# Performance work log

Measured on AMD Instinct MI355X. Metric: run time of the kernel, lower is better.

## Reference

```python
import jax, jax.numpy as jnp
import numpy as np

B, S, H = 2, 2048, 4096
NUM_HEADS = 32
HEAD_DIM = H // NUM_HEADS  # 128
ROPE_BASE = 10000.0


def _apply_rope(x, positions):
    # x: [B, S, nh, hd]; neox-style (half-split) rotation, rotary_dim == head_dim
    hd = x.shape[-1]
    inv_freq = 1.0 / (ROPE_BASE ** (jnp.arange(0, hd, 2, dtype=jnp.float32) / hd))  # [hd/2]
    freqs = positions[..., None].astype(jnp.float32) * inv_freq  # [B, S, hd/2]
    cos = jnp.cos(freqs)[:, :, None, :].astype(x.dtype)
    sin = jnp.sin(freqs)[:, :, None, :].astype(x.dtype)
    x1, x2 = jnp.split(x, 2, axis=-1)
    return jnp.concatenate([x1 * cos - x2 * sin, x2 * cos + x1 * sin], axis=-1)


def setup_inputs() -> dict:
    key = jax.random.key(0)
    k1, k2, k3 = jax.random.split(key, 3)
    hidden_states = jax.random.normal(k1, (B, S, H), dtype=jnp.float32) * 0.02
    positions = jnp.broadcast_to(jnp.arange(S, dtype=jnp.int32), (B, S))
    w_pack = jax.random.normal(k2, (3 * H, H), dtype=jnp.float32) * 0.02  # Linear(H, 3H), no bias
    w_o = jax.random.normal(k3, (H, H), dtype=jnp.float32) * 0.02        # Linear(H, H), no bias
    return {"hidden_states": hidden_states, "w_pack": w_pack, "w_o": w_o, "positions": positions}


def reference(hidden_states, w_pack, w_o, positions):
    b, s, h = hidden_states.shape
    nh, hd = NUM_HEADS, HEAD_DIM
    # fused QKV projection (W_pack)
    qkv = hidden_states @ w_pack.T  # [B, S, 3H]
    q, k, v = jnp.split(qkv, 3, axis=-1)
    q = q.reshape(b, s, nh, hd)
    k = k.reshape(b, s, nh, hd)
    v = v.reshape(b, s, nh, hd)
    # RoPE on q and k
    q = _apply_rope(q, positions)
    k = _apply_rope(k, positions)
    # causal scaled-dot-product attention (prefill over full KV cache)
    scale = 1.0 / jnp.sqrt(jnp.asarray(hd, dtype=q.dtype))
    scores = jnp.einsum('bqhd,bkhd->bhqk', q, k) * scale  # [B, nh, S, S]
    causal = jnp.tril(jnp.ones((s, s), dtype=bool))
    neg = jnp.asarray(jnp.finfo(scores.dtype).min, dtype=scores.dtype)
    scores = jnp.where(causal[None, None], scores, neg)
    attn = jax.nn.softmax(scores, axis=-1)
    out = jnp.einsum('bhqk,bkhd->bqhd', attn, v).reshape(b, s, h)
    # output projection
    return out @ w_o.T
```

## Files before the change

### kernel.cpp

```cpp
#include <hip/hip_runtime.h>
#include <hip/hip_bf16.h>
#include <math.h>

#define B_    2
#define S_    2048
#define H_    4096
#define NH_   32
#define HD_   128
#define MTOK_ (B_ * S_)
#define QKVN_ (3 * H_)

using bf16_t = __hip_bfloat16;
typedef __bf16 bf16x8 __attribute__((ext_vector_type(8)));
typedef unsigned short u16x8 __attribute__((ext_vector_type(8)));
typedef float f32x4 __attribute__((ext_vector_type(4)));

#define ASYNC_COPY16(g, l)                                                     \
  __builtin_amdgcn_global_load_lds(                                            \
      (__attribute__((address_space(1))) void*)(g),                            \
      (__attribute__((address_space(3))) void*)(l), 16, 0, 0)

static __device__ __forceinline__ f32x4 mfma16x16(bf16x8 a, bf16x8 b, f32x4 c) {
  return __builtin_amdgcn_mfma_f32_16x16x32_bf16(a, b, c, 0, 0, 0);
}

static __device__ __forceinline__ float bits_to_f(unsigned short v) {
  union { unsigned int u; float f; } cv;
  cv.u = ((unsigned int)v) << 16;
  return cv.f;
}

#define GBAR()                                                                 \
  do {                                                                         \
    __builtin_amdgcn_s_barrier();                                              \
    __builtin_amdgcn_sched_barrier(0);                                         \
  } while (0)

#define LGKM0()                                                                \
  do {                                                                         \
    asm volatile("s_waitcnt lgkmcnt(0)" ::: "memory");                         \
    __builtin_amdgcn_sched_barrier(0);                                         \
  } while (0)

__global__ void bh_detect(const unsigned short* __restrict__ p,
                          int* __restrict__ flag) {
  __shared__ float red[4];
  float m = 0.f;
  const int tid = threadIdx.x;
  for (int i = tid; i < 65536; i += 256) {
    const float f = fabsf(bits_to_f(p[i]));
    m = fmaxf(m, f);
  }
  for (int off = 1; off < 64; off <<= 1) m = fmaxf(m, __shfl_xor(m, off, 64));
  if ((tid & 63) == 0) red[tid >> 6] = m;
  __syncthreads();
  if (tid == 0) {
    const float mm = fmaxf(fmaxf(red[0], red[1]), fmaxf(red[2], red[3]));
    *flag = (mm > 1.0f) ? 1 : 0;
  }
}

__global__ __launch_bounds__(256)
void bh_convert(const void* __restrict__ src, bf16_t* __restrict__ dst,
                long n8, const int* __restrict__ flag) {
  const int isf = *flag;
  const long stride = (long)gridDim.x * 256;
  long i = (long)blockIdx.x * 256 + threadIdx.x;
  if (isf) {
    const f32x4* s = (const f32x4*)src;
    for (; i < n8; i += stride) {
      const f32x4 f0 = s[2 * i];
      const f32x4 f1 = s[2 * i + 1];
      bf16x8 o;
      o[0] = (__bf16)f0[0]; o[1] = (__bf16)f0[1];
      o[2] = (__bf16)f0[2]; o[3] = (__bf16)f0[3];
      o[4] = (__bf16)f1[0]; o[5] = (__bf16)f1[1];
      o[6] = (__bf16)f1[2]; o[7] = (__bf16)f1[3];
      *reinterpret_cast<bf16x8*>(dst + i * 8) = o;
    }
  } else {
    const u16x8* s = (const u16x8*)src;
    for (; i < n8; i += stride)
      reinterpret_cast<u16x8*>(dst)[i] = s[i];
  }
}

static __device__ __forceinline__ void stage32(const float* __restrict__ g,
                                               bf16_t* __restrict__ l) {
  const f32x4 f0 = *reinterpret_cast<const f32x4*>(g);
  const f32x4 f1 = *reinterpret_cast<const f32x4*>(g + 4);
  bf16x8 o;
  o[0] = (__bf16)f0[0]; o[1] = (__bf16)f0[1];
  o[2] = (__bf16)f0[2]; o[3] = (__bf16)f0[3];
  o[4] = (__bf16)f1[0]; o[5] = (__bf16)f1[1];
  o[6] = (__bf16)f1[2]; o[7] = (__bf16)f1[3];
  *reinterpret_cast<bf16x8*>(l) = o;
}

template <int AMODE, int BMODE, int CMODE>
__global__ __launch_bounds__(256, 2)
void bh_gemm(const void* __restrict__ Ap, int lda,
             const void* __restrict__ Bp, int ldb,
             void* __restrict__ Cp, int ldc, int N, int K,
             const int* __restrict__ flag) {
  __shared__ bf16_t As[128 * 32];
  __shared__ bf16_t Bs[128 * 32];
  const int isf = *flag;
  const bool a_f32 = AMODE && isf;
  const bool b_f32 = BMODE && isf;

  const int tid = threadIdx.x, wave = tid >> 6, lane = tid & 63;
  const int lq = lane >> 4, lc = lane & 15;
  const int m0 = blockIdx.y * 128, n0 = blockIdx.x * 128;
  const int wm = (wave >> 1) * 64, wn = (wave & 1) * 64;

  f32x4 acc[4][4] = {};

  const int srow  = wave * 16 + (lane >> 2);
  const int skoff = (lane & 3) * 8;

  const bf16_t* a16 = (const bf16_t*)Ap;
  const float*  a32 = (const float*)Ap;
  const bf16_t* b16 = (const bf16_t*)Bp;
  const float*  b32 = (const float*)Bp;

  bf16_t* lA0u = As + wave * 512;
  bf16_t* lA1u = As + 2048 + wave * 512;
  bf16_t* lB0u = Bs + wave * 512;
  bf16_t* lB1u = Bs + 2048 + wave * 512;
  bf16_t* lA0p = lA0u + lane * 8;
  bf16_t* lA1p = lA1u + lane * 8;
  bf16_t* lB0p = lB0u + lane * 8;
  bf16_t* lB1p = lB1u + lane * 8;

  const int aoff = (wm + lc) * 32 + lq * 8;
  const int boff = (wn + lc) * 32 + lq * 8;

  for (int k = 0; k < K; k += 32) {
    if (a_f32) {
      stage32(a32 + (long)(m0 + srow) * lda + skoff + k, lA0p);
      stage32(a32 + (long)(m0 + srow + 64) * lda + skoff + k, lA1p);
    } else {
      ASYNC_COPY16(a16 + (long)(m0 + srow) * lda + skoff + k, lA0u);
      ASYNC_COPY16(a16 + (long)(m0 + srow + 64) * lda + skoff + k, lA1u);
    }
    if (b_f32) {
      stage32(b32 + (long)(n0 + srow) * ldb + skoff + k, lB0p);
      stage32(b32 + (long)(n0 + srow + 64) * ldb + skoff + k, lB1p);
    } else {
      ASYNC_COPY16(b16 + (long)(n0 + srow) * ldb + skoff + k, lB0u);
      ASYNC_COPY16(b16 + (long)(n0 + srow + 64) * ldb + skoff + k, lB1u);
    }
    __syncthreads();
    bf16x8 af[4], bfr[4];
#pragma unroll
    for (int i = 0; i < 4; ++i) {
      af[i]  = *reinterpret_cast<const bf16x8*>(&As[aoff + i * 512]);
      bfr[i] = *reinterpret_cast<const bf16x8*>(&Bs[boff + i * 512]);
    }
#pragma unroll
    for (int mi = 0; mi < 4; ++mi)
#pragma unroll
      for (int ni = 0; ni < 4; ++ni)
        acc[mi][ni] = mfma16x16(af[mi], bfr[ni], acc[mi][ni]);
    __syncthreads();
  }

  const bool c_f32 = CMODE && isf;
#pragma unroll
  for (int mi = 0; mi < 4; ++mi)
#pragma unroll
    for (int ni = 0; ni < 4; ++ni)
#pragma unroll
      for (int i = 0; i < 4; ++i) {
        const long row = m0 + wm + mi * 16 + lq * 4 + i;
        const long col = n0 + wn + ni * 16 + lc;
        const float v = acc[mi][ni][i];
        if (c_f32)
          ((float*)Cp)[row * ldc + col] = v;
        else
          ((bf16_t*)Cp)[row * ldc + col] = __float2bfloat16(v);
      }
}

template <int CMODE>
__global__ __launch_bounds__(512, 2)
void bh_gemm2(const bf16_t* __restrict__ Ap, int lda,
              const bf16_t* __restrict__ Bp, int ldb,
              void* __restrict__ Cp, int ldc, int K,
              const int* __restrict__ flag) {
  __shared__ bf16_t As[2][2][128 * 64];
  __shared__ bf16_t Bs[2][2][128 * 64];
  const int isf = *flag;

  const int tid = threadIdx.x, wave = tid >> 6, lane = tid & 63;
  const int lq = lane >> 4, lc = lane & 15;
  const int wm2 = wave >> 2;
  const int wn4 = wave & 3;

  const int nbx = gridDim.x;
  int bid = blockIdx.y * nbx + blockIdx.x;
  const int cpx = (nbx * gridDim.y) >> 3;
  bid = (bid & 7) * cpx + (bid >> 3);
  const int m0 = (bid / nbx) * 256, n0 = (bid % nbx) * 256;
  const int NT = K >> 6;

  const int srow = wave * 16 + (lane >> 3);
  const int gcol = ((lane & 7) ^ (lane >> 3)) * 8;
  const int lbase = wave * 1024;

  f32x4 acc[8][4] = {};
  bf16x8 aA[2][4];
  bf16x8 bB[2][2][2];

  auto stageA = [&](int tau, int h) {
    if (tau >= NT) return;
    const bf16_t* g = Ap + (long)(m0 + h * 128 + srow) * lda + tau * 64 + gcol;
    bf16_t* l = &As[tau & 1][h][lbase];
    ASYNC_COPY16(g, l);
    ASYNC_COPY16(g + (long)8 * lda, l + 512);
  };
  auto stageB = [&](int tau, int h) {
    if (tau >= NT) return;
    const bf16_t* g = Bp + (long)(n0 + h * 128 + srow) * ldb + tau * 64 + gcol;
    bf16_t* l = &Bs[tau & 1][h][lbase];
    ASYNC_COPY16(g, l);
    ASYNC_COPY16(g + (long)8 * ldb, l + 512);
  };
  auto ldA = [&](int buf, int h) {
#pragma unroll
    for (int ks = 0; ks < 2; ++ks)
#pragma unroll
      for (int f = 0; f < 4; ++f) {
        const int row = wm2 * 64 + f * 16 + lc;
        aA[ks][f] = *reinterpret_cast<const bf16x8*>(
            &As[buf][h][row * 64 + (((ks * 4 + lq) ^ (row & 7)) * 8)]);
      }
  };
  auto ldB = [&](int buf, int h, bf16x8 (&dst)[2][2]) {
#pragma unroll
    for (int ks = 0; ks < 2; ++ks)
#pragma unroll
      for (int g = 0; g < 2; ++g) {
        const int row = wn4 * 32 + g * 16 + lc;
        dst[ks][g] = *reinterpret_cast<const bf16x8*>(
            &Bs[buf][h][row * 64 + (((ks * 4 + lq) ^ (row & 7)) * 8)]);
      }
  };

#define MMA_QUAD(qm, qn)                                                       \
  do {                                                                         \
    __builtin_amdgcn_s_setprio(1);                                             \
    _Pragma("unroll") for (int f = 0; f < 4; ++f) {                            \
      _Pragma("unroll") for (int g = 0; g < 2; ++g) {                          \
        f32x4 c = acc[(qm) * 4 + f][(qn) * 2 + g];                             \
        c = mfma16x16(aA[0][f], bB[qn][0][g], c);                              \
        c = mfma16x16(aA[1][f], bB[qn][1][g], c);                              \
        acc[(qm) * 4 + f][(qn) * 2 + g] = c;                                   \
      }                                                                        \
    }                                                                          \
    __builtin_amdgcn_s_setprio(0);                                             \
  } while (0)

  stageA(0, 0); stageB(0, 0); stageB(0, 1); stageA(0, 1);
  stageA(1, 0); stageB(1, 0); stageB(1, 1);
  asm volatile("s_waitcnt vmcnt(6)" ::: "memory");
  GBAR();

  for (int T = 0; T < NT; ++T) {
    const int buf = T & 1;
    ldA(buf, 0);
    ldB(buf, 0, bB[0]);
    stageA(T + 1, 1);
    asm volatile("s_waitcnt lgkmcnt(8)" ::: "memory");
    GBAR();
    LGKM0();
    MMA_QUAD(0, 0);
    GBAR();
    ldB(buf, 1, bB[1]);
    stageA(T + 2, 0);
    GBAR();
    LGKM0();
    MMA_QUAD(0, 1);
    GBAR();
    ldA(buf, 1);
    stageB(T + 2, 0);
    GBAR();
    LGKM0();
    MMA_QUAD(1, 1);
    GBAR();
    stageB(T + 2, 1);
    if (T + 2 < NT)
      asm volatile("s_waitcnt vmcnt(6)" ::: "memory");
    else
      asm volatile("s_waitcnt vmcnt(0)" ::: "memory");
    GBAR();
    MMA_QUAD(1, 0);
    GBAR();
  }

  const bool c_f32 = CMODE && isf;
#pragma unroll
  for (int mi = 0; mi < 8; ++mi)
#pragma unroll
    for (int ni = 0; ni < 4; ++ni)
#pragma unroll
      for (int i = 0; i < 4; ++i) {
        const long row =
            m0 + (mi >> 2) * 128 + wm2 * 64 + (mi & 3) * 16 + lq * 4 + i;
        const long col =
            n0 + (ni >> 1) * 128 + wn4 * 32 + (ni & 1) * 16 + lc;
        const float v = acc[mi][ni][i];
        if (c_f32)
          ((float*)Cp)[row * ldc + col] = v;
        else
          ((bf16_t*)Cp)[row * ldc + col] = __float2bfloat16(v);
      }
}

__global__ void bh_rope(bf16_t* __restrict__ qkv, const int* __restrict__ pos) {
  const int idx = blockIdx.x * 256 + threadIdx.x;
  const int d = idx & 63;
  const int h = (idx >> 6) & (NH_ - 1);
  const int m = idx >> 11;
  if (m >= MTOK_) return;
  const float p = (float)pos[m];
  const float inv_freq = 1.0f / powf(10000.0f, (float)d * (1.0f / 64.0f));
  float sn, cs;
  sincosf(p * inv_freq, &sn, &cs);
  bf16_t* q  = qkv + (long)m * QKVN_ + h * HD_;
  bf16_t* kk = q + H_;
  const float q1 = __bfloat162float(q[d]);
  const float q2 = __bfloat162float(q[d + 64]);
  q[d]      = __float2bfloat16(q1 * cs - q2 * sn);
  q[d + 64] = __float2bfloat16(q2 * cs + q1 * sn);
  const float k1 = __bfloat162float(kk[d]);
  const float k2 = __bfloat162float(kk[d + 64]);
  kk[d]      = __float2bfloat16(k1 * cs - k2 * sn);
  kk[d + 64] = __float2bfloat16(k2 * cs + k1 * sn);
}

__global__ void bh_transpose_v(const bf16_t* __restrict__ qkv,
                               bf16_t* __restrict__ vt) {
  __shared__ unsigned short tile[128][65];
  const int t0 = blockIdx.x * 64;
  const int h  = blockIdx.y;
  const int b  = blockIdx.z;
  const int tid = threadIdx.x;
#pragma unroll
  for (int pass = 0; pass < 4; ++pass) {
    const int row = (tid >> 4) + pass * 16;
    const int dc  = (tid & 15) * 8;
    const u16x8 v = *reinterpret_cast<const u16x8*>(
        qkv + (long)(b * S_ + t0 + row) * QKVN_ + 2 * H_ + h * HD_ + dc);
#pragma unroll
    for (int j = 0; j < 8; ++j) tile[dc + j][row] = v[j];
  }
  __syncthreads();
#pragma unroll
  for (int pass = 0; pass < 4; ++pass) {
    const int d  = (tid >> 3) + pass * 32;
    const int tc = (tid & 7) * 8;
    u16x8 o;
#pragma unroll
    for (int j = 0; j < 8; ++j) o[j] = tile[d][tc + j];
    *reinterpret_cast<u16x8*>(
        vt + ((long)(b * NH_ + h) * HD_ + d) * S_ + t0 + tc) = o;
  }
}

__global__ __launch_bounds__(512)
void bh_flash(bf16_t* __restrict__ qkv, const bf16_t* __restrict__ vt) {
  __shared__ bf16_t Ks[2][64 * 128];
  __shared__ bf16_t Vs[2][128 * 64];
  __shared__ bf16_t Ps[256 * 64];
  const int idx = blockIdx.x;
  const int qt = (S_ / 256 - 1) - (idx >> 6);
  const int bh = idx & 63;
  const int b  = bh >> 5;
  const int h  = bh & (NH_ - 1);
  const int tid = threadIdx.x, wave = tid >> 6, lane = tid & 63;
  const int lq = lane >> 4, lc = lane & 15;
  const int wrow = wave * 32;
  const float scale = 0.088388347648318447f;

  bf16x8 qf[2][4];
#pragma unroll
  for (int mt = 0; mt < 2; ++mt) {
    const bf16_t* qp =
        qkv + (long)(b * S_ + qt * 256 + wrow + mt * 16 + lc) * QKVN_ +
        h * HD_ + lq * 8;
#pragma unroll
    for (int ks = 0; ks < 4; ++ks)
      qf[mt][ks] = *reinterpret_cast<const bf16x8*>(qp + ks * 32);
  }

  f32x4 o_acc[2][8] = {};
  float m_st[2][4], l_st[2][4];
#pragma unroll
  for (int mt = 0; mt < 2; ++mt)
#pragma unroll
    for (int i = 0; i < 4; ++i) { m_st[mt][i] = -1e30f; l_st[mt][i] = 0.f; }

  auto stage = [&](int kt, int bsel) {
    const int t0 = kt * 64;
#pragma unroll
    for (int j = 0; j < 2; ++j) {
      const int p = wave * 2 + j;
      const int trow = p * 4 + (lane >> 4);
      const int kcs  = ((lane & 15) ^ (trow & 7)) * 8;
      ASYNC_COPY16(qkv + (long)(b * S_ + t0 + trow) * QKVN_ + H_ + h * HD_ + kcs,
                   &Ks[bsel][p * 512]);
      const int vrow = p * 8 + (lane >> 3);
      const int tcs  = ((lane & 7) ^ (lane >> 3)) * 8;
      ASYNC_COPY16(vt + ((long)(b * NH_ + h) * HD_ + vrow) * S_ + t0 + tcs,
                   &Vs[bsel][p * 512]);
    }
  };

  const int ktiles = 4 * qt + 4;
  stage(0, 0);

  for (int kt = 0; kt < ktiles; ++kt) {
    const int cur = kt & 1;
    if (kt + 1 < ktiles) {
      stage(kt + 1, cur ^ 1);
      asm volatile("s_waitcnt vmcnt(4)" ::: "memory");
    } else {
      asm volatile("s_waitcnt vmcnt(0)" ::: "memory");
    }
    GBAR();

    const int t0 = kt * 64;
    f32x4 sa[2][4] = {};
    __builtin_amdgcn_s_setprio(1);
#pragma unroll
    for (int ks = 0; ks < 4; ++ks) {
      bf16x8 bb[4];
#pragma unroll
      for (int nt = 0; nt < 4; ++nt)
        bb[nt] = *reinterpret_cast<const bf16x8*>(
            &Ks[cur][(nt * 16 + lc) * 128 +
                     ((ks * 32 + lq * 8) ^ ((lc & 7) << 3))]);
#pragma unroll
      for (int mt = 0; mt < 2; ++mt)
#pragma unroll
        for (int nt = 0; nt < 4; ++nt)
          sa[mt][nt] = mfma16x16(qf[mt][ks], bb[nt], sa[mt][nt]);
    }
    __builtin_amdgcn_s_setprio(0);

#pragma unroll
    for (int mt = 0; mt < 2; ++mt) {
#pragma unroll
      for (int i = 0; i < 4; ++i) {
        const int qg = qt * 256 + wrow + mt * 16 + lq * 4 + i;
        float sv[4];
        float mloc = -1e30f;
#pragma unroll
        for (int nt = 0; nt < 4; ++nt) {
          float v = sa[mt][nt][i] * scale;
          if (t0 + nt * 16 + lc > qg) v = -1e30f;
          sv[nt] = v;
          mloc = fmaxf(mloc, v);
        }
#pragma unroll
        for (int off = 1; off < 16; off <<= 1)
          mloc = fmaxf(mloc, __shfl_xor(mloc, off, 64));
        const float mnew = fmaxf(m_st[mt][i], mloc);
        const float alpha = __expf(m_st[mt][i] - mnew);
        float rsum = 0.f;
        const int psw = ((lq * 4 + i) & 7) << 3;
#pragma unroll
        for (int nt = 0; nt < 4; ++nt) {
          const float pp = __expf(sv[nt] - mnew);
          rsum += pp;
          Ps[(wrow + mt * 16 + lq * 4 + i) * 64 + ((nt * 16 + lc) ^ psw)] =
              __float2bfloat16(pp);
        }
#pragma unroll
        for (int off = 1; off < 16; off <<= 1)
          rsum += __shfl_xor(rsum, off, 64);
        l_st[mt][i] = l_st[mt][i] * alpha + rsum;
        m_st[mt][i] = mnew;
#pragma unroll
        for (int nt = 0; nt < 8; ++nt) o_acc[mt][nt][i] *= alpha;
      }
    }

    __builtin_amdgcn_s_setprio(1);
#pragma unroll
    for (int ks = 0; ks < 2; ++ks) {
      bf16x8 pa[2];
#pragma unroll
      for (int mt = 0; mt < 2; ++mt)
        pa[mt] = *reinterpret_cast<const bf16x8*>(
            &Ps[(wrow + mt * 16 + lc) * 64 +
                ((ks * 32 + lq * 8) ^ ((lc & 7) << 3))]);
#pragma unroll
      for (int nt = 0; nt < 8; ++nt) {
        const bf16x8 vb = *reinterpret_cast<const bf16x8*>(
            &Vs[cur][(nt * 16 + lc) * 64 +
                     ((ks * 32 + lq * 8) ^ ((lc & 7) << 3))]);
#pragma unroll
        for (int mt = 0; mt < 2; ++mt)
          o_acc[mt][nt] = mfma16x16(pa[mt], vb, o_acc[mt][nt]);
      }
    }
    __builtin_amdgcn_s_setprio(0);
    GBAR();
  }

#pragma unroll
  for (int mt = 0; mt < 2; ++mt)
#pragma unroll
    for (int i = 0; i < 4; ++i) {
      const float inv_l = 1.0f / l_st[mt][i];
      bf16_t* op =
          qkv + (long)(b * S_ + qt * 256 + wrow + mt * 16 + lq * 4 + i) * QKVN_ +
          h * HD_ + lc;
#pragma unroll
      for (int nt = 0; nt < 8; ++nt)
        op[nt * 16] = __float2bfloat16(o_acc[mt][nt][i] * inv_l);
    }
}

extern "C" void kernel_launch(void* const* d_in, const int* in_sizes, int n_in,
                              void* d_out, int out_size, void* d_ws,
                              size_t ws_size, hipStream_t stream) {
  const int* pos = (const int*)d_in[3];

  char* ws = (char*)d_ws;
  bf16_t* qkv  = (bf16_t*)ws;
  const size_t QKV_B = (size_t)MTOK_ * QKVN_ * 2;
  int*    flag = (int*)(ws + QKV_B);
  bf16_t* vt   = (bf16_t*)d_out;

  const size_t off  = QKV_B + 512;
  const size_t WP_B = (size_t)QKVN_ * H_ * 2;
  const size_t WO_B = (size_t)H_ * H_ * 2;
  const size_t A_B  = (size_t)MTOK_ * H_ * 2;
  const bool cvtWP = ws_size >= off + WP_B;
  const bool cvtWO = ws_size >= off + WP_B + WO_B;
  const bool cvtA  = ws_size >= off + WP_B + WO_B + A_B;
  bf16_t* wpb = (bf16_t*)(ws + off);
  bf16_t* wob = (bf16_t*)(ws + off + WP_B);
  bf16_t* abf = (bf16_t*)(ws + off + WP_B + WO_B);

  bh_detect<<<dim3(1), dim3(256), 0, stream>>>(
      (const unsigned short*)d_in[1], flag);

  if (cvtWP)
    bh_convert<<<dim3(2048), dim3(256), 0, stream>>>(
        d_in[1], wpb, (long)QKVN_ * H_ / 8, flag);
  if (cvtWO)
    bh_convert<<<dim3(2048), dim3(256), 0, stream>>>(
        d_in[2], wob, (long)H_ * H_ / 8, flag);
  if (cvtA)
    bh_convert<<<dim3(2048), dim3(256), 0, stream>>>(
        d_in[0], abf, (long)MTOK_ * H_ / 8, flag);

  if (cvtA)
    bh_gemm2<0><<<dim3(QKVN_ / 256, MTOK_ / 256), dim3(512), 0, stream>>>(
        abf, H_, wpb, H_, qkv, QKVN_, H_, flag);
  else if (cvtWP)
    bh_gemm<1, 0, 0><<<dim3(QKVN_ / 128, MTOK_ / 128), dim3(256), 0, stream>>>(
        d_in[0], H_, wpb, H_, qkv, QKVN_, QKVN_, H_, flag);
  else
    bh_gemm<1, 1, 0><<<dim3(QKVN_ / 128, MTOK_ / 128), dim3(256), 0, stream>>>(
        d_in[0], H_, d_in[1], H_, qkv, QKVN_, QKVN_, H_, flag);

  bh_rope<<<dim3((MTOK_ * NH_ * 64) / 256), dim3(256), 0, stream>>>(qkv, pos);
  bh_transpose_v<<<dim3(S_ / 64, NH_, B_), dim3(256), 0, stream>>>(qkv, vt);
  bh_flash<<<dim3((S_ / 256) * NH_ * B_), dim3(512), 0, stream>>>(qkv, vt);

  if (cvtWO)
    bh_gemm2<1><<<dim3(H_ / 256, MTOK_ / 256), dim3(512), 0, stream>>>(
        qkv, QKVN_, wob, H_, d_out, H_, H_, flag);
  else
    bh_gemm<0, 1, 1><<<dim3(H_ / 128, MTOK_ / 128), dim3(256), 0, stream>>>(
        qkv, QKVN_, d_in[2], H_, d_out, H_, H_, H_, flag);
}
```

Baseline: 1.189 ms.

## Use exp2 softmax with lazy rescaling and deferred row-sum reduction in flash attention

The flash-attention softmax now folds log2(e) into the score scale and uses the hardware v_exp_f32 (exp2) instruction instead of __expf. Rescaling of the running output and sum is skipped unless some lane's new max exceeds the stored max by more than 8 (log2 units). Each lane keeps a partial row sum, and the cross-lane shuffle reduction runs once at the end instead of every tile. Separately, the GEMM drops its block-index swizzle and uses a plain blockIdx mapping, which may hurt L2 locality. The lazy rescaling lets probabilities reach up to 2^8 before rounding to bf16, which carries some numerical risk.

```diff
diff --git a/kernel.cpp b/kernel.cpp
--- a/kernel.cpp
+++ b/kernel.cpp
@@ -28,6 +28,12 @@
   union { unsigned int u; float f; } cv;
   cv.u = ((unsigned int)v) << 16;
   return cv.f;
+}
+
+static __device__ __forceinline__ float exp2_hw(float x) {
+  float r;
+  asm("v_exp_f32 %0, %1" : "=v"(r) : "v"(x));
+  return r;
 }
 
 #define GBAR()                                                                 \
@@ -197,12 +203,7 @@
   const int lq = lane >> 4, lc = lane & 15;
   const int wm2 = wave >> 2;
   const int wn4 = wave & 3;
-
-  const int nbx = gridDim.x;
-  int bid = blockIdx.y * nbx + blockIdx.x;
-  const int cpx = (nbx * gridDim.y) >> 3;
-  bid = (bid & 7) * cpx + (bid >> 3);
-  const int m0 = (bid / nbx) * 256, n0 = (bid % nbx) * 256;
+  const int m0 = blockIdx.y * 256, n0 = blockIdx.x * 256;
   const int NT = K >> 6;
 
   const int srow = wave * 16 + (lane >> 3);
@@ -382,7 +383,7 @@
   const int tid = threadIdx.x, wave = tid >> 6, lane = tid & 63;
   const int lq = lane >> 4, lc = lane & 15;
   const int wrow = wave * 32;
-  const float scale = 0.088388347648318447f;
+  const float scale2 = 0.12751744f;
 
   bf16x8 qf[2][4];
 #pragma unroll
@@ -459,7 +460,7 @@
         float mloc = -1e30f;
 #pragma unroll
         for (int nt = 0; nt < 4; ++nt) {
-          float v = sa[mt][nt][i] * scale;
+          float v = sa[mt][nt][i] * scale2;
           if (t0 + nt * 16 + lc > qg) v = -1e30f;
           sv[nt] = v;
           mloc = fmaxf(mloc, v);
@@ -467,24 +468,25 @@
 #pragma unroll
         for (int off = 1; off < 16; off <<= 1)
           mloc = fmaxf(mloc, __shfl_xor(mloc, off, 64));
-        const float mnew = fmaxf(m_st[mt][i], mloc);
-        const float alpha = __expf(m_st[mt][i] - mnew);
+        if (!__all(mloc - m_st[mt][i] <= 8.0f)) {
+          const float mnew = fmaxf(m_st[mt][i], mloc);
+          const float alpha = exp2_hw(m_st[mt][i] - mnew);
+          l_st[mt][i] *= alpha;
+#pragma unroll
+          for (int nt = 0; nt < 8; ++nt) o_acc[mt][nt][i] *= alpha;
+          m_st[mt][i] = mnew;
+        }
+        const float mcur = m_st[mt][i];
         float rsum = 0.f;
         const int psw = ((lq * 4 + i) & 7) << 3;
 #pragma unroll
         for (int nt = 0; nt < 4; ++nt) {
-          const float pp = __expf(sv[nt] - mnew);
+          const float pp = exp2_hw(sv[nt] - mcur);
           rsum += pp;
           Ps[(wrow + mt * 16 + lq * 4 + i) * 64 + ((nt * 16 + lc) ^ psw)] =
               __float2bfloat16(pp);
         }
-#pragma unroll
-        for (int off = 1; off < 16; off <<= 1)
-          rsum += __shfl_xor(rsum, off, 64);
-        l_st[mt][i] = l_st[mt][i] * alpha + rsum;
-        m_st[mt][i] = mnew;
-#pragma unroll
-        for (int nt = 0; nt < 8; ++nt) o_acc[mt][nt][i] *= alpha;
+        l_st[mt][i] += rsum;
       }
     }
 
@@ -515,7 +517,10 @@
   for (int mt = 0; mt < 2; ++mt)
 #pragma unroll
     for (int i = 0; i < 4; ++i) {
-      const float inv_l = 1.0f / l_st[mt][i];
+      float l = l_st[mt][i];
+#pragma unroll
+      for (int off = 1; off < 16; off <<= 1) l += __shfl_xor(l, off, 64);
+      const float inv_l = 1.0f / l;
       bf16_t* op =
           qkv + (long)(b * S_ + qt * 256 + wrow + mt * 16 + lq * 4 + i) * QKVN_ +
           h * HD_ + lc;
```

Result: faster. 1.146 ms (-3.6%).
